# Kernel optimization log

Hardware: AMD Instinct MI355X
Metric: run time of the kernel (lower is better)

Reference implementation:

```python
import jax, jax.numpy as jnp
import numpy as np

CONTEXT = 10  # symmetric_mask default; self.context is NOT used in call()
SCALE = 16.0  # hard-coded divisor in the source
NEG = 1e9


def setup_inputs() -> dict:
    key = jax.random.key(0)
    k1, k2, k3, k4 = jax.random.split(key, 4)
    B, N, D = 2, 4096, 512
    H, dh = 8, 64
    x = jax.random.normal(k1, (B, N, D), dtype=jnp.float32)
    Wq = jax.random.normal(k2, (H, D, dh), dtype=jnp.float32) * 1e-4
    Wv = jax.random.normal(k3, (H, D, dh), dtype=jnp.float32) * 1e-4
    Wup = jax.random.normal(k4, (H * dh, D), dtype=jnp.float32) * 1e-4
    return {"x": x, "Wq": Wq, "Wv": Wv, "Wup": Wup}


def reference(x, Wq, Wv, Wup):
    B, N, D = x.shape
    H, _, dh = Wq.shape
    # Per-head projections (no bias), vectorized over heads
    Q = jnp.einsum('bnd,hdk->bhnk', x, Wq)  # [B,H,N,dh]
    V = jnp.einsum('bnd,hdk->bhnk', x, Wv)  # [B,H,N,dh]
    # Full score matrix Q @ V^T / 16 (V doubles as keys in this module)
    scores = jnp.einsum('bhnk,bhmk->bhnm', Q, V) / SCALE  # [B,H,N,N]
    # Symmetric band mask: |i-j| <= CONTEXT and |i-j| > 0 (diagonal excluded)
    idx = jnp.arange(N)
    diff = jnp.abs(idx[:, None] - idx[None, :])
    mask = (diff <= CONTEXT) & (diff > 0)  # [N,N]
    scores = scores - NEG * (~mask).astype(scores.dtype)
    weights = jax.nn.softmax(scores, axis=-1)
    C = jnp.einsum('bhnm,bhmk->bhnk', weights, V)  # [B,H,N,dh]
    heads = C.transpose(0, 2, 1, 3).reshape(B, N, H * dh)  # concat heads
    return heads @ Wup  # [B,N,D]
```

## Files before the change

### kernel.cpp

```cpp
#include <hip/hip_runtime.h>
#include <math.h>

#define N_TOK 4096
#define DMODEL 512
#define NHEAD 8
#define DHEAD 64
#define CTX 10
#define NROW 8192

typedef __bf16 bf16x4 __attribute__((ext_vector_type(4)));
typedef __bf16 bf16x8 __attribute__((ext_vector_type(8)));
typedef float  f32x4  __attribute__((ext_vector_type(4)));

#define GLOAD_LDS16(g, l) __builtin_amdgcn_global_load_lds(                 \
    (const __attribute__((address_space(1))) void*)(g),                     \
    (__attribute__((address_space(3))) void*)(l), 16, 0, 0)

__global__ __launch_bounds__(256) void conv_w(const float* __restrict__ Wq,
                                              const float* __restrict__ Wv,
                                              const float* __restrict__ Wup,
                                              const float* __restrict__ x,
                                              __bf16* __restrict__ Wtqv,
                                              __bf16* __restrict__ Wtup,
                                              __bf16* __restrict__ xb)
{
    const int tid = threadIdx.x;
    const int bid = blockIdx.x;

    if (bid >= 192) {
        const int b3 = bid - 192;
        const float* src = x + (size_t)b3 * 16384;
        __bf16* dst = xb + (size_t)b3 * 16384;
#pragma unroll
        for (int it = 0; it < 16; it++) {
            const int idx = it * 1024 + tid * 4;
            const float4 v = *(const float4*)(src + idx);
            bf16x4 o;
            o[0] = (__bf16)v.x; o[1] = (__bf16)v.y;
            o[2] = (__bf16)v.z; o[3] = (__bf16)v.w;
            *(bf16x4*)(dst + idx) = o;
        }
        return;
    }

    __shared__ float T[64][65];

    const float* src;
    __bf16* dstBase;
    int k0, rowBase, srcStride;
    if (bid < 128) {
        k0 = (bid & 7) * 64;
        const int h   = (bid >> 3) & 7;
        const int mat = bid >> 6;
        src = (mat ? Wv : Wq) + (size_t)h * DMODEL * DHEAD;
        dstBase = Wtqv;
        rowBase = mat * 512 + h * 64;
        srcStride = DHEAD;
    } else {
        const int b2 = bid - 128;
        k0 = (b2 & 7) * 64;
        const int n0 = (b2 >> 3) * 64;
        src = Wup + n0;
        dstBase = Wtup;
        rowBase = n0;
        srcStride = DMODEL;
    }

#pragma unroll
    for (int it = 0; it < 4; it++) {
        const int kr = it * 16 + (tid >> 4);
        const int c4 = (tid & 15) * 4;
        const float4 v = *(const float4*)(src + (size_t)(k0 + kr) * srcStride + c4);
        T[kr][c4 + 0] = v.x; T[kr][c4 + 1] = v.y;
        T[kr][c4 + 2] = v.z; T[kr][c4 + 3] = v.w;
    }
    __syncthreads();
    const int c   = tid >> 2;
    const int kk0 = (tid & 3) * 16;
    __bf16* dst = dstBase + (size_t)(rowBase + c) * DMODEL + k0 + kk0;
    bf16x8 o0, o1;
#pragma unroll
    for (int j = 0; j < 8; j++) o0[j] = (__bf16)T[kk0 + j][c];
#pragma unroll
    for (int j = 0; j < 8; j++) o1[j] = (__bf16)T[kk0 + 8 + j][c];
    *(bf16x8*)dst = o0;
    *(bf16x8*)(dst + 8) = o1;
}

__global__ __launch_bounds__(256) void gemm_qv_mfma(
    const __bf16* __restrict__ xb,
    const __bf16* __restrict__ Wt,
    __bf16* __restrict__ Qt,
    __bf16* __restrict__ Vt)
{
    __shared__ __align__(16) __bf16 As[128 * 64];
    __shared__ __align__(16) __bf16 Bs[64 * 64];

    const int tid  = threadIdx.x;
    const int w    = tid >> 6;
    const int lane = tid & 63;
    const int lm   = lane & 15;
    const int q    = lane >> 4;
    const int bid  = blockIdx.x;
    const int row0 = (bid & 63) * 128;
    const int col0 = (bid >> 6) * 64;

    const int sxr = lane >> 3;
    const int sxc = ((lane & 7) ^ sxr) * 8;
    const __bf16* gA = xb + (size_t)(row0 + w * 32 + sxr) * DMODEL + sxc;
    const __bf16* gB = Wt + (size_t)(col0 + w * 16 + sxr) * DMODEL + sxc;
    __bf16* lA = As + w * 32 * 64;
    __bf16* lB = Bs + w * 16 * 64;

    const int off0 = ((q ^ (lm & 7)) * 8);

    f32x4 acc[2][4];
#pragma unroll
    for (int i = 0; i < 2; i++)
#pragma unroll
        for (int j = 0; j < 4; j++) acc[i][j] = (f32x4){0.f, 0.f, 0.f, 0.f};

    for (int k0 = 0; k0 < DMODEL; k0 += 64) {
        __syncthreads();
#pragma unroll
        for (int g = 0; g < 4; g++)
            GLOAD_LDS16(gA + (size_t)g * 8 * DMODEL, lA + g * 512);
#pragma unroll
        for (int g = 0; g < 2; g++)
            GLOAD_LDS16(gB + (size_t)g * 8 * DMODEL, lB + g * 512);
        gA += 64; gB += 64;
        __syncthreads();

        bf16x8 af[2][2], bfr[4][2];
#pragma unroll
        for (int mi = 0; mi < 2; mi++) {
            const int r = (w * 32 + mi * 16 + lm) * 64;
            af[mi][0] = *(const bf16x8*)&As[r + off0];
            af[mi][1] = *(const bf16x8*)&As[r + (off0 ^ 32)];
        }
#pragma unroll
        for (int ni = 0; ni < 4; ni++) {
            const int r = (ni * 16 + lm) * 64;
            bfr[ni][0] = *(const bf16x8*)&Bs[r + off0];
            bfr[ni][1] = *(const bf16x8*)&Bs[r + (off0 ^ 32)];
        }
#pragma unroll
        for (int kk2 = 0; kk2 < 2; kk2++)
#pragma unroll
            for (int mi = 0; mi < 2; mi++)
#pragma unroll
                for (int ni = 0; ni < 4; ni++)
                    acc[mi][ni] = __builtin_amdgcn_mfma_f32_16x16x32_bf16(
                        af[mi][kk2], bfr[ni][kk2], acc[mi][ni], 0, 0, 0);
    }

#pragma unroll
    for (int ni = 0; ni < 4; ni++) {
        const int c  = col0 + ni * 16 + lm;
        const int cc = c & 511;
        __bf16* outB = (c < 512 ? Qt : Vt);
#pragma unroll
        for (int mi = 0; mi < 2; mi++) {
            const int m  = row0 + w * 32 + mi * 16 + q * 4;
            const int bb = m >> 12;
            const int nt = m & (N_TOK - 1);
            bf16x4 o;
            o[0] = (__bf16)acc[mi][ni][0];
            o[1] = (__bf16)acc[mi][ni][1];
            o[2] = (__bf16)acc[mi][ni][2];
            o[3] = (__bf16)acc[mi][ni][3];
            *(bf16x4*)(outB + ((size_t)(bb * 512 + cc)) * N_TOK + nt) = o;
        }
    }
}

#define VSTRIDE 97
__global__ __launch_bounds__(256) void attn_band(
    const __bf16* __restrict__ Qt,
    const __bf16* __restrict__ Vt,
    __bf16* __restrict__ Hb16)
{
    __shared__ float Vs[64 * VSTRIDE];

    const int tid  = threadIdx.x;
    const int bh   = blockIdx.x >> 6;
    const int tile = blockIdx.x & 63;
    const int i0   = tile * 64;
    const int b    = bh >> 3;
    const int h    = bh & 7;

    const __bf16* vband = Vt + (size_t)bh * DHEAD * N_TOK;
    const int tok0 = i0 - 16;
#pragma unroll
    for (int it = 0; it < 3; it++) {
        const int idx = it * 256 + tid;
        const int k   = idx / 12;
        const int s8  = idx - k * 12;
        const int tokg = tok0 + s8 * 8;
        const int tokc = min(max(tokg, 0), N_TOK - 8);
        const bf16x8 v = *(const bf16x8*)(vband + (size_t)k * N_TOK + tokc);
        float* dst = &Vs[k * VSTRIDE + s8 * 8];
#pragma unroll
        for (int e = 0; e < 8; e++) dst[e] = (float)v[e];
    }

    const int lane = tid & 63;
    const int wv   = tid >> 6;
    const int il   = lane & 15;
    const int p    = lane >> 4;
    const int i    = i0 + wv * 16 + il;
    const int slot0 = wv * 16 + il + 6;

    const __bf16* qbase = Qt + ((size_t)bh * DHEAD + p * 16) * N_TOK;
    float qv[16];
#pragma unroll
    for (int k = 0; k < 16; k++) qv[k] = (float)qbase[(size_t)k * N_TOK + i];

    __syncthreads();

    float c[16];
#pragma unroll
    for (int k = 0; k < 16; k++) c[k] = 0.f;
    float Z = 0.f;

#pragma unroll 3
    for (int d = 0; d < 2 * CTX + 1; d++) {
        const float* vrow = &Vs[p * 16 * VSTRIDE + slot0 + d];
        float v[16];
#pragma unroll
        for (int k = 0; k < 16; k++) v[k] = vrow[k * VSTRIDE];
        float s = 0.f;
#pragma unroll
        for (int k = 0; k < 16; k++) s += qv[k] * v[k];
        s += __shfl_xor(s, 16, 64);
        s += __shfl_xor(s, 32, 64);

        const int j = i + d - CTX;
        const bool valid = (d != CTX) && (j >= 0) && (j < N_TOK);
        const float w = valid ? __expf(s * 0.0625f) : 0.f;
        Z += w;
#pragma unroll
        for (int k = 0; k < 16; k++) c[k] += w * v[k];
    }

    const float inv = 1.f / Z;
    __bf16* dst = Hb16 + ((size_t)(b * N_TOK + i)) * DMODEL + h * DHEAD + p * 16;
    bf16x8 o0, o1;
#pragma unroll
    for (int k = 0; k < 8; k++) o0[k] = (__bf16)(c[k] * inv);
#pragma unroll
    for (int k = 0; k < 8; k++) o1[k] = (__bf16)(c[8 + k] * inv);
    *(bf16x8*)dst = o0;
    *(bf16x8*)(dst + 8) = o1;
}

__global__ __launch_bounds__(256) void gemm_out_mfma(
    const __bf16* __restrict__ Hb,
    const __bf16* __restrict__ Wt,
    float* __restrict__ out)
{
    __shared__ __align__(16) __bf16 As[128 * 64];
    __shared__ __align__(16) __bf16 Bs[64 * 64];

    const int tid  = threadIdx.x;
    const int w    = tid >> 6;
    const int lane = tid & 63;
    const int lm   = lane & 15;
    const int q    = lane >> 4;
    const int bid  = blockIdx.x;
    const int row0 = (bid & 63) * 128;
    const int col0 = (bid >> 6) * 64;

    const int sxr = lane >> 3;
    const int sxc = ((lane & 7) ^ sxr) * 8;
    const __bf16* gA = Hb + (size_t)(row0 + w * 32 + sxr) * DMODEL + sxc;
    const __bf16* gB = Wt + (size_t)(col0 + w * 16 + sxr) * DMODEL + sxc;
    __bf16* lA = As + w * 32 * 64;
    __bf16* lB = Bs + w * 16 * 64;

    const int off0 = ((q ^ (lm & 7)) * 8);

    f32x4 acc[2][4];
#pragma unroll
    for (int i = 0; i < 2; i++)
#pragma unroll
        for (int j = 0; j < 4; j++) acc[i][j] = (f32x4){0.f, 0.f, 0.f, 0.f};

    for (int k0 = 0; k0 < DMODEL; k0 += 64) {
        __syncthreads();
#pragma unroll
        for (int g = 0; g < 4; g++)
            GLOAD_LDS16(gA + (size_t)g * 8 * DMODEL, lA + g * 512);
#pragma unroll
        for (int g = 0; g < 2; g++)
            GLOAD_LDS16(gB + (size_t)g * 8 * DMODEL, lB + g * 512);
        gA += 64; gB += 64;
        __syncthreads();

        bf16x8 af[2][2], bfr[4][2];
#pragma unroll
        for (int mi = 0; mi < 2; mi++) {
            const int r = (w * 32 + mi * 16 + lm) * 64;
            af[mi][0] = *(const bf16x8*)&As[r + off0];
            af[mi][1] = *(const bf16x8*)&As[r + (off0 ^ 32)];
        }
#pragma unroll
        for (int ni = 0; ni < 4; ni++) {
            const int r = (ni * 16 + lm) * 64;
            bfr[ni][0] = *(const bf16x8*)&Bs[r + off0];
            bfr[ni][1] = *(const bf16x8*)&Bs[r + (off0 ^ 32)];
        }
#pragma unroll
        for (int kk2 = 0; kk2 < 2; kk2++)
#pragma unroll
            for (int mi = 0; mi < 2; mi++)
#pragma unroll
                for (int ni = 0; ni < 4; ni++)
                    acc[mi][ni] = __builtin_amdgcn_mfma_f32_16x16x32_bf16(
                        af[mi][kk2], bfr[ni][kk2], acc[mi][ni], 0, 0, 0);
    }

#pragma unroll
    for (int mi = 0; mi < 2; mi++) {
        const int m0 = row0 + w * 32 + mi * 16 + q * 4;
#pragma unroll
        for (int ni = 0; ni < 4; ni++) {
            const int n = col0 + ni * 16 + lm;
#pragma unroll
            for (int r = 0; r < 4; r++)
                out[(size_t)(m0 + r) * DMODEL + n] = acc[mi][ni][r];
        }
    }
}

extern "C" void kernel_launch(void* const* d_in, const int* in_sizes, int n_in,
                              void* d_out, int out_size, void* d_ws, size_t ws_size,
                              hipStream_t stream)
{
    const float* x   = (const float*)d_in[0];
    const float* Wq  = (const float*)d_in[1];
    const float* Wv  = (const float*)d_in[2];
    const float* Wup = (const float*)d_in[3];
    float* out = (float*)d_out;

    const size_t QV = (size_t)2 * NHEAD * N_TOK * DHEAD;
    __bf16* Qt   = (__bf16*)d_ws;
    __bf16* Vt   = Qt + QV;
    __bf16* Hb16 = Vt + QV;
    __bf16* Wtqv = Hb16 + (size_t)NROW * DMODEL;
    __bf16* Wtup = Wtqv + (size_t)1024 * DMODEL;
    __bf16* xb   = Wtup + (size_t)512 * DMODEL;

    dim3 blk(256);
    conv_w       <<<dim3(448),  blk, 0, stream>>>(Wq, Wv, Wup, x, Wtqv, Wtup, xb);
    gemm_qv_mfma <<<dim3(1024), blk, 0, stream>>>(xb, Wtqv, Qt, Vt);
    attn_band    <<<dim3(1024), blk, 0, stream>>>(Qt, Vt, Hb16);
    gemm_out_mfma<<<dim3(512),  blk, 0, stream>>>(Hb16, Wtup, out);
}
```

Measured before the change: 114.9 us.

## Double-buffer GEMM LDS tiles and transpose attention V tile to token-major

Both bf16 MFMA GEMMs now keep two LDS buffers and issue the next k-tile's global-to-LDS loads before computing on the current tile, with one barrier per iteration instead of two. This is meant to overlap load latency with MFMA work. The attention kernel's shared V tile becomes token-major (row stride 68 floats), so each lane reads its 16 V values as four float4 LDS loads instead of strided scalar loads. In exchange the staging loop does scalar gathers across dh rows, and the GEMMs use twice the LDS, which may reduce occupancy.

```diff
diff --git a/kernel.cpp b/kernel.cpp
--- a/kernel.cpp
+++ b/kernel.cpp
@@ -93,8 +93,8 @@
     __bf16* __restrict__ Qt,
     __bf16* __restrict__ Vt)
 {
-    __shared__ __align__(16) __bf16 As[128 * 64];
-    __shared__ __align__(16) __bf16 Bs[64 * 64];
+    __shared__ __align__(16) __bf16 As[2 * 128 * 64];
+    __shared__ __align__(16) __bf16 Bs[2 * 64 * 64];
 
     const int tid  = threadIdx.x;
     const int w    = tid >> 6;
@@ -114,33 +114,41 @@
 
     const int off0 = ((q ^ (lm & 7)) * 8);
 
+#define STAGE_QV(buf, kk) do {                                              \
+    _Pragma("unroll")                                                       \
+    for (int g = 0; g < 4; g++)                                             \
+        GLOAD_LDS16(gA + (kk) + (size_t)g * 8 * DMODEL,                     \
+                    lA + (buf) * 8192 + g * 512);                           \
+    _Pragma("unroll")                                                       \
+    for (int g = 0; g < 2; g++)                                             \
+        GLOAD_LDS16(gB + (kk) + (size_t)g * 8 * DMODEL,                     \
+                    lB + (buf) * 4096 + g * 512);                           \
+} while (0)
+
     f32x4 acc[2][4];
 #pragma unroll
     for (int i = 0; i < 2; i++)
 #pragma unroll
         for (int j = 0; j < 4; j++) acc[i][j] = (f32x4){0.f, 0.f, 0.f, 0.f};
 
-    for (int k0 = 0; k0 < DMODEL; k0 += 64) {
-        __syncthreads();
-#pragma unroll
-        for (int g = 0; g < 4; g++)
-            GLOAD_LDS16(gA + (size_t)g * 8 * DMODEL, lA + g * 512);
-#pragma unroll
-        for (int g = 0; g < 2; g++)
-            GLOAD_LDS16(gB + (size_t)g * 8 * DMODEL, lB + g * 512);
-        gA += 64; gB += 64;
-        __syncthreads();
+    STAGE_QV(0, 0);
+    __syncthreads();
+
+#pragma unroll
+    for (int t = 0; t < 8; t++) {
+        const int cur = t & 1;
+        if (t < 7) STAGE_QV(cur ^ 1, (t + 1) * 64);
 
         bf16x8 af[2][2], bfr[4][2];
 #pragma unroll
         for (int mi = 0; mi < 2; mi++) {
-            const int r = (w * 32 + mi * 16 + lm) * 64;
+            const int r = cur * 8192 + (w * 32 + mi * 16 + lm) * 64;
             af[mi][0] = *(const bf16x8*)&As[r + off0];
             af[mi][1] = *(const bf16x8*)&As[r + (off0 ^ 32)];
         }
 #pragma unroll
         for (int ni = 0; ni < 4; ni++) {
-            const int r = (ni * 16 + lm) * 64;
+            const int r = cur * 4096 + (ni * 16 + lm) * 64;
             bfr[ni][0] = *(const bf16x8*)&Bs[r + off0];
             bfr[ni][1] = *(const bf16x8*)&Bs[r + (off0 ^ 32)];
         }
@@ -152,7 +160,9 @@
                 for (int ni = 0; ni < 4; ni++)
                     acc[mi][ni] = __builtin_amdgcn_mfma_f32_16x16x32_bf16(
                         af[mi][kk2], bfr[ni][kk2], acc[mi][ni], 0, 0, 0);
-    }
+        __syncthreads();
+    }
+#undef STAGE_QV
 
 #pragma unroll
     for (int ni = 0; ni < 4; ni++) {
@@ -174,13 +184,13 @@
     }
 }
 
-#define VSTRIDE 97
+#define VROW 68
 __global__ __launch_bounds__(256) void attn_band(
     const __bf16* __restrict__ Qt,
     const __bf16* __restrict__ Vt,
     __bf16* __restrict__ Hb16)
 {
-    __shared__ float Vs[64 * VSTRIDE];
+    __shared__ float Vs[96 * VROW];
 
     const int tid  = threadIdx.x;
     const int bh   = blockIdx.x >> 6;
@@ -194,14 +204,18 @@
 #pragma unroll
     for (int it = 0; it < 3; it++) {
         const int idx = it * 256 + tid;
-        const int k   = idx / 12;
-        const int s8  = idx - k * 12;
-        const int tokg = tok0 + s8 * 8;
-        const int tokc = min(max(tokg, 0), N_TOK - 8);
-        const bf16x8 v = *(const bf16x8*)(vband + (size_t)k * N_TOK + tokc);
-        float* dst = &Vs[k * VSTRIDE + s8 * 8];
-#pragma unroll
-        for (int e = 0; e < 8; e++) dst[e] = (float)v[e];
+        const int g   = idx & 7;
+        const int s   = idx >> 3;
+        const int tokg = tok0 + s;
+        const int tokc = min(max(tokg, 0), N_TOK - 1);
+        float f[8];
+#pragma unroll
+        for (int e = 0; e < 8; e++)
+            f[e] = (float)vband[(size_t)(g * 8 + e) * N_TOK + tokc];
+        float4 f0 = {f[0], f[1], f[2], f[3]};
+        float4 f1 = {f[4], f[5], f[6], f[7]};
+        *(float4*)&Vs[s * VROW + g * 8 + 0] = f0;
+        *(float4*)&Vs[s * VROW + g * 8 + 4] = f1;
     }
 
     const int lane = tid & 63;
@@ -225,10 +239,11 @@
 
 #pragma unroll 3
     for (int d = 0; d < 2 * CTX + 1; d++) {
-        const float* vrow = &Vs[p * 16 * VSTRIDE + slot0 + d];
+        const float* vrow = &Vs[(slot0 + d) * VROW + p * 16];
         float v[16];
 #pragma unroll
-        for (int k = 0; k < 16; k++) v[k] = vrow[k * VSTRIDE];
+        for (int jj = 0; jj < 4; jj++)
+            *(float4*)&v[jj * 4] = *(const float4*)&vrow[jj * 4];
         float s = 0.f;
 #pragma unroll
         for (int k = 0; k < 16; k++) s += qv[k] * v[k];
@@ -259,8 +274,8 @@
     const __bf16* __restrict__ Wt,
     float* __restrict__ out)
 {
-    __shared__ __align__(16) __bf16 As[128 * 64];
-    __shared__ __align__(16) __bf16 Bs[64 * 64];
+    __shared__ __align__(16) __bf16 As[2 * 128 * 64];
+    __shared__ __align__(16) __bf16 Bs[2 * 64 * 64];
 
     const int tid  = threadIdx.x;
     const int w    = tid >> 6;
@@ -280,33 +295,41 @@
 
     const int off0 = ((q ^ (lm & 7)) * 8);
 
+#define STAGE_OUT(buf, kk) do {                                             \
+    _Pragma("unroll")                                                       \
+    for (int g = 0; g < 4; g++)                                             \
+        GLOAD_LDS16(gA + (kk) + (size_t)g * 8 * DMODEL,                     \
+                    lA + (buf) * 8192 + g * 512);                           \
+    _Pragma("unroll")                                                       \
+    for (int g = 0; g < 2; g++)                                             \
+        GLOAD_LDS16(gB + (kk) + (size_t)g * 8 * DMODEL,                     \
+                    lB + (buf) * 4096 + g * 512);                           \
+} while (0)
+
     f32x4 acc[2][4];
 #pragma unroll
     for (int i = 0; i < 2; i++)
 #pragma unroll
         for (int j = 0; j < 4; j++) acc[i][j] = (f32x4){0.f, 0.f, 0.f, 0.f};
 
-    for (int k0 = 0; k0 < DMODEL; k0 += 64) {
-        __syncthreads();
-#pragma unroll
-        for (int g = 0; g < 4; g++)
-            GLOAD_LDS16(gA + (size_t)g * 8 * DMODEL, lA + g * 512);
-#pragma unroll
-        for (int g = 0; g < 2; g++)
-            GLOAD_LDS16(gB + (size_t)g * 8 * DMODEL, lB + g * 512);
-        gA += 64; gB += 64;
-        __syncthreads();
+    STAGE_OUT(0, 0);
+    __syncthreads();
+
+#pragma unroll
+    for (int t = 0; t < 8; t++) {
+        const int cur = t & 1;
+        if (t < 7) STAGE_OUT(cur ^ 1, (t + 1) * 64);
 
         bf16x8 af[2][2], bfr[4][2];
 #pragma unroll
         for (int mi = 0; mi < 2; mi++) {
-            const int r = (w * 32 + mi * 16 + lm) * 64;
+            const int r = cur * 8192 + (w * 32 + mi * 16 + lm) * 64;
             af[mi][0] = *(const bf16x8*)&As[r + off0];
             af[mi][1] = *(const bf16x8*)&As[r + (off0 ^ 32)];
         }
 #pragma unroll
         for (int ni = 0; ni < 4; ni++) {
-            const int r = (ni * 16 + lm) * 64;
+            const int r = cur * 4096 + (ni * 16 + lm) * 64;
             bfr[ni][0] = *(const bf16x8*)&Bs[r + off0];
             bfr[ni][1] = *(const bf16x8*)&Bs[r + (off0 ^ 32)];
         }
@@ -318,7 +341,9 @@
                 for (int ni = 0; ni < 4; ni++)
                     acc[mi][ni] = __builtin_amdgcn_mfma_f32_16x16x32_bf16(
                         af[mi][kk2], bfr[ni][kk2], acc[mi][ni], 0, 0, 0);
-    }
+        __syncthreads();
+    }
+#undef STAGE_OUT
 
 #pragma unroll
     for (int mi = 0; mi < 2; mi++) {
```

After: 119.4 us. 1.04x slower.
